# Kernel optimization log

Hardware: AMD Instinct MI355X
Metric: run time of the kernel (lower is better)

## Reference

```python
import jax, jax.numpy as jnp
import numpy as np

B, T, C, H = 4, 2048, 768, 64

def setup_inputs() -> dict:
    key = jax.random.key(0)
    kx, kq, kk, kv = jax.random.split(key, 4)
    x = jax.random.normal(kx, (B, T, C), dtype=jnp.float32)
    # torch Linear(C->H, bias=False): y = x @ W with W [C, H]
    s = 1.0 / np.sqrt(C)
    Wq = jax.random.normal(kq, (C, H), dtype=jnp.float32) * s
    Wk = jax.random.normal(kk, (C, H), dtype=jnp.float32) * s
    Wv = jax.random.normal(kv, (C, H), dtype=jnp.float32) * s
    return {"x": x, "Wq": Wq, "Wk": Wk, "Wv": Wv}

def reference(x, Wq, Wk, Wv):
    Bx, Tx, Cx = x.shape
    q = jnp.einsum('btc,ch->bth', x, Wq)
    k = jnp.einsum('btc,ch->bth', x, Wk)
    v = jnp.einsum('btc,ch->bth', x, Wv)
    # NOTE: original scales by C**-0.5 (n_embeddings), not head_size**-0.5
    w = jnp.einsum('bqh,bkh->bqk', q, k) * (Cx ** -0.5)  # [B, T, T]
    causal = jnp.tril(jnp.ones((Tx, Tx), dtype=bool))
    w = jnp.where(causal, w, -jnp.inf)
    w = jax.nn.softmax(w, axis=-1)
    # dropout: eval mode (identity)
    out = jnp.einsum('bqk,bkh->bqh', w, v)  # [B, T, H]
    return out
```

## Files before the change

### kernel.cpp

```cpp
#include <hip/hip_runtime.h>
#include <math.h>

#define TB 2048
#define CB 768
#define NB 4
#define NROWS (NB * TB)
#define SKV 6
#define NSMAX 32
#define WGPB 528

typedef __attribute__((ext_vector_type(8))) short bf16x8;
typedef __attribute__((ext_vector_type(4))) float f32x4;
typedef __attribute__((ext_vector_type(2))) float f32x2;
typedef __attribute__((ext_vector_type(2))) unsigned int u32x2;
typedef __attribute__((ext_vector_type(4))) unsigned int u32x4;

__device__ inline unsigned short f2bf(float f) {
  union { float f; unsigned u; } v; v.f = f;
  unsigned r = v.u + 0x7FFFu + ((v.u >> 16) & 1u);
  return (unsigned short)(r >> 16);
}
__device__ inline unsigned pack2bf(float a, float b) {
  return (unsigned)f2bf(a) | ((unsigned)f2bf(b) << 16);
}
__device__ inline float bf2f(unsigned short u) {
  union { unsigned u; float f; } v; v.u = (unsigned)u << 16; return v.f;
}

__global__ void cvt_w_kernel(const float* __restrict__ Wq, const float* __restrict__ Wk,
                             const float* __restrict__ Wv, unsigned short* __restrict__ Wt) {
  __shared__ float tw[64][65];
  const float* W = (blockIdx.y == 0) ? Wq : (blockIdx.y == 1) ? Wk : Wv;
  const int c0 = blockIdx.x * 64;
  const int row = threadIdx.x >> 2, seg = threadIdx.x & 3;
#pragma unroll
  for (int i = 0; i < 4; ++i) {
    float4 f = *(const float4*)(W + (size_t)(c0 + row) * 64 + seg * 16 + i * 4);
    tw[row][seg * 16 + i * 4 + 0] = f.x;
    tw[row][seg * 16 + i * 4 + 1] = f.y;
    tw[row][seg * 16 + i * 4 + 2] = f.z;
    tw[row][seg * 16 + i * 4 + 3] = f.w;
  }
  __syncthreads();
  const int j = threadIdx.x >> 2, cq = threadIdx.x & 3;
  unsigned short* dst = Wt + (size_t)(blockIdx.y * 64 + j) * CB + c0 + cq * 16;
  u32x4 ua, ub;
#pragma unroll
  for (int i = 0; i < 4; ++i) ua[i] = pack2bf(tw[cq * 16 + 2 * i][j], tw[cq * 16 + 2 * i + 1][j]);
#pragma unroll
  for (int i = 0; i < 4; ++i) ub[i] = pack2bf(tw[cq * 16 + 8 + 2 * i][j], tw[cq * 16 + 9 + 2 * i][j]);
  *(u32x4*)dst = ua;
  *(u32x4*)(dst + 8) = ub;
}

__launch_bounds__(256)
__global__ void proj_kernel(const float* __restrict__ x, const unsigned short* __restrict__ Wt,
                            unsigned short* __restrict__ part, int ksteps) {
  __shared__ __align__(16) unsigned short xs[64 * 64];
  const int tid = threadIdx.x;
  const int wv = tid >> 6;
  const int l = tid & 63;
  const int lrow = l & 15, lg = l >> 4;
  const int m0 = blockIdx.x * 64;
  const int ks = blockIdx.y;
  const int kbase = ks * ksteps * 64;
  const int srow = tid >> 2;
  const int sq = tid & 3;
  const float* xp = x + (size_t)(m0 + srow) * CB + sq * 16;

  f32x4 acc[4][3];
#pragma unroll
  for (int a = 0; a < 4; ++a)
#pragma unroll
    for (int n = 0; n < 3; ++n) acc[a][n] = (f32x4){0.f, 0.f, 0.f, 0.f};

  for (int kk = 0; kk < ksteps; ++kk) {
    int k0 = kbase + kk * 64;
    bf16x8 c0, c1;
#pragma unroll
    for (int i = 0; i < 2; ++i) {
      float4 f = *(const float4*)(xp + k0 + 4 * i);
      c0[4 * i + 0] = (short)f2bf(f.x); c0[4 * i + 1] = (short)f2bf(f.y);
      c0[4 * i + 2] = (short)f2bf(f.z); c0[4 * i + 3] = (short)f2bf(f.w);
    }
#pragma unroll
    for (int i = 0; i < 2; ++i) {
      float4 f = *(const float4*)(xp + k0 + 8 + 4 * i);
      c1[4 * i + 0] = (short)f2bf(f.x); c1[4 * i + 1] = (short)f2bf(f.y);
      c1[4 * i + 2] = (short)f2bf(f.z); c1[4 * i + 3] = (short)f2bf(f.w);
    }
    {
      char* base = (char*)xs + srow * 128;
      int swz = (srow & 7) << 4;
      *(bf16x8*)(base + ((sq * 32 + 0) ^ swz)) = c0;
      *(bf16x8*)(base + ((sq * 32 + 16) ^ swz)) = c1;
    }
    __syncthreads();

#pragma unroll
    for (int s = 0; s < 2; ++s) {
      bf16x8 af[4], bfr[3];
#pragma unroll
      for (int mf = 0; mf < 4; ++mf) {
        int r = mf * 16 + lrow;
        af[mf] = *(const bf16x8*)((const char*)xs + r * 128 +
                                  ((s * 64 + lg * 16) ^ ((r & 7) << 4)));
      }
#pragma unroll
      for (int nf = 0; nf < 3; ++nf) {
        int col = wv * 48 + nf * 16 + lrow;
        bfr[nf] = *(const bf16x8*)(Wt + (size_t)col * CB + k0 + s * 32 + lg * 8);
      }
#pragma unroll
      for (int mf = 0; mf < 4; ++mf)
#pragma unroll
        for (int nf = 0; nf < 3; ++nf)
          acc[mf][nf] = __builtin_amdgcn_mfma_f32_16x16x32_bf16(af[mf], bfr[nf], acc[mf][nf], 0, 0, 0);
    }
    __syncthreads();
  }

  unsigned short* pb = part + (size_t)ks * NROWS * 192;
#pragma unroll
  for (int mf = 0; mf < 4; ++mf)
#pragma unroll
    for (int nf = 0; nf < 3; ++nf)
#pragma unroll
      for (int r = 0; r < 4; ++r) {
        int grow = m0 + mf * 16 + lg * 4 + r;
        int j = wv * 48 + nf * 16 + lrow;
        pb[(size_t)grow * 192 + j] = f2bf(acc[mf][nf][r]);
      }
}

__global__ void reduce_qkv_kernel(const unsigned short* __restrict__ part,
                                  unsigned short* __restrict__ q, unsigned short* __restrict__ k,
                                  unsigned short* __restrict__ vT, int SK) {
  __shared__ float tr[64][17];
  if (blockIdx.x < 4096) {
    int id = blockIdx.x * 256 + threadIdx.x;
    int row = id >> 7, col = id & 127;
    float s = 0.f;
    for (int ks = 0; ks < SK; ++ks)
      s += bf2f(part[((size_t)ks * NROWS + row) * 192 + col]);
    unsigned short v = f2bf(s);
    if (col < 64) q[(size_t)row * 64 + col] = v;
    else          k[(size_t)row * 64 + (col - 64)] = v;
  } else {
    int bid = blockIdx.x - 4096;
    const int t0 = (bid & 127) * 16;
    const int b = bid >> 7;
    const int c = threadIdx.x & 63, trow = threadIdx.x >> 6;
#pragma unroll
    for (int p = 0; p < 4; ++p) {
      int tl = p * 4 + trow;
      int row = b * TB + t0 + tl;
      float s = 0.f;
      for (int ks = 0; ks < SK; ++ks)
        s += bf2f(part[((size_t)ks * NROWS + row) * 192 + 128 + c]);
      tr[c][tl] = s;
    }
    __syncthreads();
    const int h = threadIdx.x >> 2, tq = threadIdx.x & 3;
    u32x2 pk;
    pk.x = pack2bf(tr[h][tq * 4 + 0], tr[h][tq * 4 + 1]);
    pk.y = pack2bf(tr[h][tq * 4 + 2], tr[h][tq * 4 + 3]);
    *(u32x2*)(vT + ((size_t)(b * 64 + h)) * TB + t0 + tq * 4) = pk;
  }
}

__launch_bounds__(256)
__global__ void attn_kernel(const unsigned short* __restrict__ q,
                            const unsigned short* __restrict__ k,
                            const unsigned short* __restrict__ vT,
                            unsigned short* __restrict__ PO, float* __restrict__ Mp,
                            float* __restrict__ Lp) {
  __shared__ __align__(16) char ksm[8192];
  __shared__ __align__(16) char vsm[8192];
  const int tid = threadIdx.x;
  const int wid = tid >> 6, l = tid & 63;
  const int lrow = l & 15, lg = l >> 4;
  const int b = blockIdx.y;
  const int w = blockIdx.x;

  int g = (int)((sqrtf((float)(8 * w + 1)) - 1.f) * 0.5f);
  while ((g + 1) * (g + 2) / 2 <= w) ++g;
  while (g * (g + 1) / 2 > w) --g;
  const int blk = w - g * (g + 1) / 2;
  const int kv0 = blk * 64;
  const bool last = (blk == g);
  const int qrow = (4 * g + wid) * 16 + lrow;

  const unsigned short* qb = q + (size_t)b * TB * 64;
  const char* kbb = (const char*)(k + (size_t)b * TB * 64);
  const unsigned short* vb = vT + (size_t)b * 64 * TB;

  const int srow = tid >> 2;
  const int sc = (tid & 3) * 32;
  float4 kg0 = *(const float4*)(kbb + (size_t)kv0 * 128 + tid * 32);
  float4 kg1 = *(const float4*)(kbb + (size_t)kv0 * 128 + tid * 32 + 16);
  const char* vrow = (const char*)(vb + (size_t)srow * TB + kv0);
  float4 vg0 = *(const float4*)(vrow + sc);
  float4 vg1 = *(const float4*)(vrow + sc + 16);

  bf16x8 qf[2];
#pragma unroll
  for (int s = 0; s < 2; ++s)
    qf[s] = *(const bf16x8*)(qb + (size_t)qrow * 64 + s * 32 + lg * 8);

  {
    const int kswz_w = (srow & 7) << 4;
    *(float4*)(ksm + srow * 128 + ((sc + 0) ^ kswz_w)) = kg0;
    *(float4*)(ksm + srow * 128 + ((sc + 16) ^ kswz_w)) = kg1;
    const int vswz_w = (srow & 3) << 5;
    *(float4*)(vsm + srow * 128 + ((sc + 0) ^ vswz_w)) = vg0;
    *(float4*)(vsm + srow * 128 + ((sc + 16) ^ vswz_w)) = vg1;
  }
  __syncthreads();

  const int kswz = (lrow & 7) << 4;
  f32x4 S[4];
#pragma unroll
  for (int cf = 0; cf < 4; ++cf) S[cf] = (f32x4){0.f, 0.f, 0.f, 0.f};
#pragma unroll
  for (int cf = 0; cf < 4; ++cf) {
    const char* kp = ksm + (cf * 16 + lrow) * 128;
#pragma unroll
    for (int s = 0; s < 2; ++s) {
      bf16x8 kf = *(const bf16x8*)(kp + ((s * 64 + lg * 16) ^ kswz));
      S[cf] = __builtin_amdgcn_mfma_f32_16x16x32_bf16(kf, qf[s], S[cf], 0, 0, 0);
    }
  }

  const float scale = 0.03608439182435161f;
  float tmx = -INFINITY;
#pragma unroll
  for (int cf = 0; cf < 4; ++cf)
#pragma unroll
    for (int r = 0; r < 4; ++r) {
      float vv = S[cf][r] * scale;
      if (last) {
        int kvi = kv0 + cf * 16 + lg * 4 + r;
        vv = (kvi > qrow) ? -INFINITY : vv;
      }
      S[cf][r] = vv;
      tmx = fmaxf(tmx, vv);
    }
  tmx = fmaxf(tmx, __shfl_xor(tmx, 16));
  tmx = fmaxf(tmx, __shfl_xor(tmx, 32));

  float lsl = 0.f;
  float p[4][4];
#pragma unroll
  for (int cf = 0; cf < 4; ++cf)
#pragma unroll
    for (int r = 0; r < 4; ++r) {
      float pe = __expf(S[cf][r] - tmx);
      p[cf][r] = pe;
      lsl += pe;
    }
  union { unsigned u[4]; bf16x8 v; } pbu[2];
#pragma unroll
  for (int s = 0; s < 2; ++s) {
    pbu[s].u[0] = pack2bf(p[2 * s][0], p[2 * s][1]);
    pbu[s].u[1] = pack2bf(p[2 * s][2], p[2 * s][3]);
    pbu[s].u[2] = pack2bf(p[2 * s + 1][0], p[2 * s + 1][1]);
    pbu[s].u[3] = pack2bf(p[2 * s + 1][2], p[2 * s + 1][3]);
  }

  f32x4 o[4];
#pragma unroll
  for (int hf = 0; hf < 4; ++hf) o[hf] = (f32x4){0.f, 0.f, 0.f, 0.f};
  const int rswz = (lrow & 3) << 5;
#pragma unroll
  for (int s = 0; s < 2; ++s)
#pragma unroll
    for (int hf = 0; hf < 4; ++hf) {
      int r = hf * 16 + lrow;
      int a1 = r * 128 + ((s * 64 + lg * 8) ^ rswz);
      u32x2 lo = *(const u32x2*)(vsm + a1);
      u32x2 hi = *(const u32x2*)(vsm + (a1 ^ 32));
      union { unsigned u[4]; bf16x8 v; } vfu;
      vfu.u[0] = lo.x; vfu.u[1] = lo.y; vfu.u[2] = hi.x; vfu.u[3] = hi.y;
      o[hf] = __builtin_amdgcn_mfma_f32_16x16x32_bf16(vfu.v, pbu[s].v, o[hf], 0, 0, 0);
    }

  float ls = lsl;
  ls += __shfl_xor(ls, 16);
  ls += __shfl_xor(ls, 32);

  size_t rowg = (size_t)blk * NROWS + b * TB + qrow;
  unsigned short* pop = PO + rowg * 64 + lg * 4;
#pragma unroll
  for (int hf = 0; hf < 4; ++hf) {
    u32x2 pk;
    pk.x = pack2bf(o[hf][0], o[hf][1]);
    pk.y = pack2bf(o[hf][2], o[hf][3]);
    *(u32x2*)(pop + hf * 16) = pk;
  }
  if (lg == 0) {
    Mp[rowg] = tmx;
    Lp[rowg] = ls;
  }
}

__global__ void attn_reduce_kernel(const unsigned short* __restrict__ PO,
                                   const float* __restrict__ Mp,
                                   const float* __restrict__ Lp,
                                   float* __restrict__ out) {
  int id = blockIdx.x * 256 + threadIdx.x;
  if (id >= NROWS * 32) return;
  int row = id >> 5, h0 = (id & 31) * 2;
  int t = row & (TB - 1);
  int ns = (t >> 6) + 1;
  float M = -INFINITY;
#pragma unroll 4
  for (int s = 0; s < ns; ++s) M = fmaxf(M, Mp[(size_t)s * NROWS + row]);
  float L = 0.f, a0 = 0.f, a1 = 0.f;
#pragma unroll 4
  for (int s = 0; s < ns; ++s) {
    float w = __expf(Mp[(size_t)s * NROWS + row] - M);
    L += Lp[(size_t)s * NROWS + row] * w;
    unsigned pv = *(const unsigned*)(PO + ((size_t)s * NROWS + row) * 64 + h0);
    a0 += bf2f((unsigned short)(pv & 0xffff)) * w;
    a1 += bf2f((unsigned short)(pv >> 16)) * w;
  }
  float rL = 1.f / L;
  f32x2 r; r.x = a0 * rL; r.y = a1 * rL;
  *(f32x2*)(out + (size_t)row * 64 + h0) = r;
}

extern "C" void kernel_launch(void* const* d_in, const int* in_sizes, int n_in,
                              void* d_out, int out_size, void* d_ws, size_t ws_size,
                              hipStream_t stream) {
  const float* x  = (const float*)d_in[0];
  const float* Wq = (const float*)d_in[1];
  const float* Wk = (const float*)d_in[2];
  const float* Wv = (const float*)d_in[3];
  float* out = (float*)d_out;

  unsigned short* Wt = (unsigned short*)d_ws;
  unsigned short* qb = Wt + 192 * CB;
  unsigned short* kb = qb + (size_t)NROWS * 64;
  unsigned short* vT = kb + (size_t)NROWS * 64;
  char* scratch = (char*)(vT + (size_t)NROWS * 64);

  int SK = SKV;
  unsigned short* part = (unsigned short*)scratch;
  unsigned short* PO = (unsigned short*)scratch;
  float* Mp = (float*)(scratch + (size_t)NSMAX * NROWS * 64 * 2);
  float* Lp = Mp + (size_t)NSMAX * NROWS;

  hipLaunchKernelGGL(cvt_w_kernel, dim3(12, 3), dim3(256), 0, stream,
                     Wq, Wk, Wv, Wt);
  hipLaunchKernelGGL(proj_kernel, dim3(NROWS / 64, SK), dim3(256), 0, stream,
                     x, Wt, part, CB / (64 * SK));
  hipLaunchKernelGGL(reduce_qkv_kernel, dim3(4096 + 512), dim3(256), 0, stream,
                     part, qb, kb, vT, SK);
  hipLaunchKernelGGL(attn_kernel, dim3(WGPB, NB), dim3(256), 0, stream,
                     qb, kb, vT, PO, Mp, Lp);
  hipLaunchKernelGGL(attn_reduce_kernel, dim3((NROWS * 32) / 256), dim3(256), 0, stream,
                     PO, Mp, Lp, out);
}
```

Before: 62.56 us.

## Replace split-K projection plus reduce kernel with direct full-K projection

The QKV projection no longer splits K six ways and writes bf16 partials for a separate reduce kernel. Each block now covers 16 rows over the full 768-wide K, accumulates in registers, and writes q, k and a transposed v straight from its epilogue, with a one-step register prefetch of x. This drops one kernel launch and the write and read of the partial-sum buffer. It also avoids rounding the partials to bf16 before summing. In exchange, each block has a serial loop over all of K, and W is reloaded once per 16-row tile, so W traffic rises fourfold.

```diff
diff --git a/kernel.cpp b/kernel.cpp
--- a/kernel.cpp
+++ b/kernel.cpp
@@ -5,7 +5,6 @@
 #define CB 768
 #define NB 4
 #define NROWS (NB * TB)
-#define SKV 6
 #define NSMAX 32
 #define WGPB 528
 
@@ -54,114 +53,67 @@
 }
 
 __launch_bounds__(256)
-__global__ void proj_kernel(const float* __restrict__ x, const unsigned short* __restrict__ Wt,
-                            unsigned short* __restrict__ part, int ksteps) {
-  __shared__ __align__(16) unsigned short xs[64 * 64];
+__global__ void proj_direct_kernel(const float* __restrict__ x,
+                                   const unsigned short* __restrict__ Wt,
+                                   unsigned short* __restrict__ q,
+                                   unsigned short* __restrict__ k,
+                                   unsigned short* __restrict__ vT) {
+  __shared__ __align__(16) unsigned short xs[16 * 64];
+  __shared__ float tr[64][17];
   const int tid = threadIdx.x;
   const int wv = tid >> 6;
   const int l = tid & 63;
   const int lrow = l & 15, lg = l >> 4;
-  const int m0 = blockIdx.x * 64;
-  const int ks = blockIdx.y;
-  const int kbase = ks * ksteps * 64;
-  const int srow = tid >> 2;
-  const int sq = tid & 3;
-  const float* xp = x + (size_t)(m0 + srow) * CB + sq * 16;
-
-  f32x4 acc[4][3];
-#pragma unroll
-  for (int a = 0; a < 4; ++a)
-#pragma unroll
-    for (int n = 0; n < 3; ++n) acc[a][n] = (f32x4){0.f, 0.f, 0.f, 0.f};
-
-  for (int kk = 0; kk < ksteps; ++kk) {
-    int k0 = kbase + kk * 64;
-    bf16x8 c0, c1;
-#pragma unroll
-    for (int i = 0; i < 2; ++i) {
-      float4 f = *(const float4*)(xp + k0 + 4 * i);
-      c0[4 * i + 0] = (short)f2bf(f.x); c0[4 * i + 1] = (short)f2bf(f.y);
-      c0[4 * i + 2] = (short)f2bf(f.z); c0[4 * i + 3] = (short)f2bf(f.w);
-    }
-#pragma unroll
-    for (int i = 0; i < 2; ++i) {
-      float4 f = *(const float4*)(xp + k0 + 8 + 4 * i);
-      c1[4 * i + 0] = (short)f2bf(f.x); c1[4 * i + 1] = (short)f2bf(f.y);
-      c1[4 * i + 2] = (short)f2bf(f.z); c1[4 * i + 3] = (short)f2bf(f.w);
-    }
+  const int m0 = blockIdx.x * 16;
+  const int srow = tid >> 4;
+  const int sq = tid & 15;
+  const float* xp = x + (size_t)(m0 + srow) * CB + sq * 4;
+  const int swz = (srow & 7) << 4;
+
+  f32x4 acc[3];
+#pragma unroll
+  for (int n = 0; n < 3; ++n) acc[n] = (f32x4){0.f, 0.f, 0.f, 0.f};
+
+  float4 f = *(const float4*)xp;
+  for (int k0 = 0; k0 < CB; k0 += 64) {
     {
-      char* base = (char*)xs + srow * 128;
-      int swz = (srow & 7) << 4;
-      *(bf16x8*)(base + ((sq * 32 + 0) ^ swz)) = c0;
-      *(bf16x8*)(base + ((sq * 32 + 16) ^ swz)) = c1;
-    }
+      u32x2 c;
+      c.x = pack2bf(f.x, f.y);
+      c.y = pack2bf(f.z, f.w);
+      *(u32x2*)((char*)xs + srow * 128 + ((sq * 8) ^ swz)) = c;
+    }
+    if (k0 + 64 < CB) f = *(const float4*)(xp + k0 + 64);
     __syncthreads();
 
 #pragma unroll
     for (int s = 0; s < 2; ++s) {
-      bf16x8 af[4], bfr[3];
-#pragma unroll
-      for (int mf = 0; mf < 4; ++mf) {
-        int r = mf * 16 + lrow;
-        af[mf] = *(const bf16x8*)((const char*)xs + r * 128 +
-                                  ((s * 64 + lg * 16) ^ ((r & 7) << 4)));
-      }
+      bf16x8 af = *(const bf16x8*)((const char*)xs + lrow * 128 +
+                                   ((s * 64 + lg * 16) ^ ((lrow & 7) << 4)));
 #pragma unroll
       for (int nf = 0; nf < 3; ++nf) {
         int col = wv * 48 + nf * 16 + lrow;
-        bfr[nf] = *(const bf16x8*)(Wt + (size_t)col * CB + k0 + s * 32 + lg * 8);
+        bf16x8 bfr = *(const bf16x8*)(Wt + (size_t)col * CB + k0 + s * 32 + lg * 8);
+        acc[nf] = __builtin_amdgcn_mfma_f32_16x16x32_bf16(af, bfr, acc[nf], 0, 0, 0);
       }
-#pragma unroll
-      for (int mf = 0; mf < 4; ++mf)
-#pragma unroll
-        for (int nf = 0; nf < 3; ++nf)
-          acc[mf][nf] = __builtin_amdgcn_mfma_f32_16x16x32_bf16(af[mf], bfr[nf], acc[mf][nf], 0, 0, 0);
     }
     __syncthreads();
   }
 
-  unsigned short* pb = part + (size_t)ks * NROWS * 192;
-#pragma unroll
-  for (int mf = 0; mf < 4; ++mf)
-#pragma unroll
-    for (int nf = 0; nf < 3; ++nf)
-#pragma unroll
-      for (int r = 0; r < 4; ++r) {
-        int grow = m0 + mf * 16 + lg * 4 + r;
-        int j = wv * 48 + nf * 16 + lrow;
-        pb[(size_t)grow * 192 + j] = f2bf(acc[mf][nf][r]);
-      }
-}
-
-__global__ void reduce_qkv_kernel(const unsigned short* __restrict__ part,
-                                  unsigned short* __restrict__ q, unsigned short* __restrict__ k,
-                                  unsigned short* __restrict__ vT, int SK) {
-  __shared__ float tr[64][17];
-  if (blockIdx.x < 4096) {
-    int id = blockIdx.x * 256 + threadIdx.x;
-    int row = id >> 7, col = id & 127;
-    float s = 0.f;
-    for (int ks = 0; ks < SK; ++ks)
-      s += bf2f(part[((size_t)ks * NROWS + row) * 192 + col]);
-    unsigned short v = f2bf(s);
-    if (col < 64) q[(size_t)row * 64 + col] = v;
-    else          k[(size_t)row * 64 + (col - 64)] = v;
-  } else {
-    int bid = blockIdx.x - 4096;
-    const int t0 = (bid & 127) * 16;
-    const int b = bid >> 7;
-    const int c = threadIdx.x & 63, trow = threadIdx.x >> 6;
-#pragma unroll
-    for (int p = 0; p < 4; ++p) {
-      int tl = p * 4 + trow;
-      int row = b * TB + t0 + tl;
-      float s = 0.f;
-      for (int ks = 0; ks < SK; ++ks)
-        s += bf2f(part[((size_t)ks * NROWS + row) * 192 + 128 + c]);
-      tr[c][tl] = s;
-    }
-    __syncthreads();
-    const int h = threadIdx.x >> 2, tq = threadIdx.x & 3;
+#pragma unroll
+  for (int nf = 0; nf < 3; ++nf) {
+    int j = wv * 48 + nf * 16 + lrow;
+#pragma unroll
+    for (int r = 0; r < 4; ++r) {
+      int grow = m0 + lg * 4 + r;
+      if (j < 64)       q[(size_t)grow * 64 + j] = f2bf(acc[nf][r]);
+      else if (j < 128) k[(size_t)grow * 64 + (j - 64)] = f2bf(acc[nf][r]);
+      else              tr[j - 128][lg * 4 + r] = acc[nf][r];
+    }
+  }
+  __syncthreads();
+  {
+    const int b = m0 >> 11, t0 = m0 & (TB - 1);
+    const int h = tid >> 2, tq = tid & 3;
     u32x2 pk;
     pk.x = pack2bf(tr[h][tq * 4 + 0], tr[h][tq * 4 + 1]);
     pk.y = pack2bf(tr[h][tq * 4 + 2], tr[h][tq * 4 + 3]);
@@ -345,18 +297,14 @@
   unsigned short* vT = kb + (size_t)NROWS * 64;
   char* scratch = (char*)(vT + (size_t)NROWS * 64);
 
-  int SK = SKV;
-  unsigned short* part = (unsigned short*)scratch;
   unsigned short* PO = (unsigned short*)scratch;
   float* Mp = (float*)(scratch + (size_t)NSMAX * NROWS * 64 * 2);
   float* Lp = Mp + (size_t)NSMAX * NROWS;
 
   hipLaunchKernelGGL(cvt_w_kernel, dim3(12, 3), dim3(256), 0, stream,
                      Wq, Wk, Wv, Wt);
-  hipLaunchKernelGGL(proj_kernel, dim3(NROWS / 64, SK), dim3(256), 0, stream,
-                     x, Wt, part, CB / (64 * SK));
-  hipLaunchKernelGGL(reduce_qkv_kernel, dim3(4096 + 512), dim3(256), 0, stream,
-                     part, qb, kb, vT, SK);
+  hipLaunchKernelGGL(proj_direct_kernel, dim3(NROWS / 16), dim3(256), 0, stream,
+                     x, Wt, qb, kb, vT);
   hipLaunchKernelGGL(attn_kernel, dim3(WGPB, NB), dim3(256), 0, stream,
                      qb, kb, vT, PO, Mp, Lp);
   hipLaunchKernelGGL(attn_reduce_kernel, dim3((NROWS * 32) / 256), dim3(256), 0, stream,
```

Measured after the change: 56.76 us. -9.3%, faster.
